# Optimization experiments

Hardware: AMD Instinct MI355X
Metric: run time of the kernel (lower is better)

The kernel has to match this reference:

```python
import jax, jax.numpy as jnp
import numpy as np

# Multi-resolution implicit grid layout (static, mirrors the int32 buffers
# `resolutions` / `offsets` of the torch module).
RESOLUTIONS = (16, 32, 48, 64)
LEVEL_SIZES = tuple(r ** 3 for r in RESOLUTIONS)  # offsets[l+1]-offsets[l]
N_TOTAL = sum(LEVEL_SIZES)  # 409600
B, C_IN, C_OUT, K = 4, 16, 16, 3


def setup_inputs() -> dict:
    key = jax.random.key(0)
    k1, k2, k3 = jax.random.split(key, 3)
    inp = jax.random.normal(k1, (B, N_TOTAL, C_IN), dtype=jnp.float32)
    weight = jax.random.normal(k2, (C_OUT, C_IN, K, K, K), dtype=jnp.float32) * 0.05
    bias = jax.random.normal(k3, (C_OUT,), dtype=jnp.float32) * 0.05
    return {"input": inp, "weight": weight, "bias": bias}


def reference(input, weight, bias):
    """Offset-indexed multi-resolution 3D conv.

    input:  [B, N_total, Cin] flat per-level voxel features,
            level l occupies a contiguous block of resolutions[l]**3 rows
            laid out as a dense R x R x R grid (row-major).
    weight: [Cout, Cin, k, k, k]; bias: [Cout].
    Each level is convolved independently with SAME padding (zero pad at
    level boundaries), then written back to the same flat layout.
    """
    Bv, _, Cin = input.shape
    Cout = weight.shape[0]
    outs = []
    start = 0
    for R in RESOLUTIONS:  # fixed small number of levels
        n = R ** 3
        # [B, n, Cin] -> [B, Cin, R, R, R]
        x = input[:, start:start + n, :].reshape(Bv, R, R, R, Cin)
        x = jnp.transpose(x, (0, 4, 1, 2, 3))
        y = jax.lax.conv_general_dilated(
            x, weight,
            window_strides=(1, 1, 1),
            padding='SAME',
            dimension_numbers=('NCDHW', 'OIDHW', 'NCDHW'),
        )
        y = y + bias[None, :, None, None, None]
        # back to flat layout [B, n, Cout]
        outs.append(jnp.transpose(y, (0, 2, 3, 4, 1)).reshape(Bv, n, Cout))
        start += n
    return jnp.concatenate(outs, axis=1)  # [B, N_total, Cout]
```

## Files before the change

kernel.cpp:

```cpp
#include <hip/hip_runtime.h>

#define N_TOTAL 409600

typedef short short8 __attribute__((ext_vector_type(8)));
typedef float floatx4 __attribute__((ext_vector_type(4)));

__device__ __forceinline__ unsigned short f2bf(float f) {
    unsigned u = __float_as_uint(f);
    u += 0x7fffu + ((u >> 16) & 1u);
    return (unsigned short)(u >> 16);
}

__global__ __launch_bounds__(256) void wt_pack(const float* __restrict__ w,
                                               unsigned short* __restrict__ wtf) {
    int i = blockIdx.x * 256 + threadIdx.x;
    if (i >= 7168) return;
    int j    = i & 7;
    int lane = (i >> 3) & 63;
    int p    = i >> 9;
    int q    = lane >> 4;
    int tap  = 2 * p + (q >> 1);
    int ci   = (q & 1) * 8 + j;
    int co   = lane & 15;
    float v  = (tap < 27) ? w[(co * 16 + ci) * 27 + tap] : 0.0f;
    wtf[(p * 64 + lane) * 8 + j] = f2bf(v);
}

template <int R>
__global__ __launch_bounds__(256) void pad_bf16(const float* __restrict__ in,
                                                unsigned short* __restrict__ dst,
                                                int vbase) {
    constexpr int Rp   = R + 2;
    constexpr int nPad = Rp * Rp * Rp;
    int tid = blockIdx.x * 256 + threadIdx.x;
    if (tid >= nPad * 2) return;
    int half = tid & 1;
    int p    = tid >> 1;
    int b    = blockIdx.y;
    int pw = p % Rp, ph = (p / Rp) % Rp, pd = p / (Rp * Rp);

    short8 o = {0, 0, 0, 0, 0, 0, 0, 0};
    if (pw >= 1 && pw <= R && ph >= 1 && ph <= R && pd >= 1 && pd <= R) {
        int v = (((pd - 1) * R) + (ph - 1)) * R + (pw - 1);
        const float* src = in + ((size_t)(b * N_TOTAL + vbase) + v) * 16 + half * 8;
        float4 a0 = ((const float4*)src)[0];
        float4 a1 = ((const float4*)src)[1];
        o[0] = (short)f2bf(a0.x); o[1] = (short)f2bf(a0.y);
        o[2] = (short)f2bf(a0.z); o[3] = (short)f2bf(a0.w);
        o[4] = (short)f2bf(a1.x); o[5] = (short)f2bf(a1.y);
        o[6] = (short)f2bf(a1.z); o[7] = (short)f2bf(a1.w);
    }
    *(short8*)(dst + ((size_t)b * nPad + p) * 16 + half * 8) = o;
}

template <int R>
__device__ __forceinline__ constexpr int tapOff(int t) {
    constexpr int Rp = R + 2;
    int kd = t / 9, kh = (t / 3) % 3, kw = t % 3;
    return (((kd - 1) * Rp + (kh - 1)) * Rp + (kw - 1)) * 16;
}

template <int R>
__global__ __launch_bounds__(256) void conv_mfma(const unsigned short* __restrict__ grid,
                                                 const unsigned short* __restrict__ wtf,
                                                 const float* __restrict__ bias,
                                                 float* __restrict__ out,
                                                 int vbase) {
    constexpr int Rp   = R + 2;
    constexpr int nPad = Rp * Rp * Rp;
    const int lane = threadIdx.x & 63;
    const int wave = threadIdx.x >> 6;
    const int b    = blockIdx.y;

    const int tile   = blockIdx.x * 4 + wave;
    const int voxel0 = tile * 16;
    const int d  = voxel0 / (R * R);
    const int h  = (voxel0 / R) % R;
    const int w0 = voxel0 % R;

    const int q      = lane >> 4;
    const int r      = lane & 15;
    const int tapSel = q >> 1;
    const int ciHalf = (q & 1) * 8;

    short8 bf[14];
#pragma unroll
    for (int p = 0; p < 14; ++p)
        bf[p] = *(const short8*)(wtf + (p * 64 + lane) * 8);

    const unsigned short* base =
        grid + (size_t)b * nPad * 16 +
        ((((size_t)(d + 1) * Rp + (h + 1)) * Rp + (w0 + 1)) + r) * 16 + ciHalf;

    const float bv = bias[r];
    floatx4 acc = {bv, bv, bv, bv};

#pragma unroll
    for (int p = 0; p < 14; ++p) {
        const int t1  = (2 * p + 1 < 27) ? 2 * p + 1 : 26;
        const int o0  = tapOff<R>(2 * p);
        const int o1  = tapOff<R>(t1);
        const int off = tapSel ? o1 : o0;
        short8 a = *(const short8*)(base + off);
        acc = __builtin_amdgcn_mfma_f32_16x16x32_bf16(a, bf[p], acc, 0, 0, 0);
    }

    const size_t outBase = ((size_t)b * N_TOTAL + vbase + voxel0) * 16;
#pragma unroll
    for (int j = 0; j < 4; ++j) {
        int row = q * 4 + j;
        out[outBase + (size_t)row * 16 + r] = acc[j];
    }
}

__global__ __launch_bounds__(256) void wt_transpose(const float* __restrict__ w,
                                                    float* __restrict__ wt) {
    int i = blockIdx.x * 256 + threadIdx.x;
    if (i < 6912) {
        int co = i / 432;
        int rr = i - co * 432;
        int ci = rr / 27;
        int tap = rr - ci * 27;
        wt[(tap * 16 + ci) * 16 + co] = w[i];
    }
}

template <int R>
__global__ __launch_bounds__(256) void conv_f32(const float* __restrict__ in,
                                                const float* __restrict__ wt,
                                                const float* __restrict__ bias,
                                                float* __restrict__ out, int base) {
    const int v = blockIdx.x * 256 + threadIdx.x;
    const int b = blockIdx.y;
    const int w = v % R, h = (v / R) % R, d = v / (R * R);
    const size_t lvl = ((size_t)b * N_TOTAL + base) * 16;
    const float* inp = in + lvl;
    float acc[16];
#pragma unroll
    for (int co = 0; co < 16; ++co) acc[co] = bias[co];
    for (int kd = 0; kd < 3; ++kd) {
        const int zd = d + kd - 1;
        if ((unsigned)zd >= (unsigned)R) continue;
        for (int kh = 0; kh < 3; ++kh) {
            const int zh = h + kh - 1;
            if ((unsigned)zh >= (unsigned)R) continue;
#pragma unroll
            for (int kw = 0; kw < 3; ++kw) {
                const int zw = w + kw - 1;
                if ((unsigned)zw >= (unsigned)R) continue;
                const float* src = inp + (size_t)(((zd * R + zh) * R) + zw) * 16;
                const float4* p4 = reinterpret_cast<const float4*>(src);
                float4 q0 = p4[0], q1 = p4[1], q2 = p4[2], q3 = p4[3];
                float x[16] = {q0.x, q0.y, q0.z, q0.w, q1.x, q1.y, q1.z, q1.w,
                               q2.x, q2.y, q2.z, q2.w, q3.x, q3.y, q3.z, q3.w};
                const float* wp = wt + ((kd * 3 + kh) * 3 + kw) * 256;
#pragma unroll
                for (int ci = 0; ci < 16; ++ci)
#pragma unroll
                    for (int co = 0; co < 16; ++co)
                        acc[co] = fmaf(x[ci], wp[ci * 16 + co], acc[co]);
            }
        }
    }
    float* dst = out + lvl + (size_t)v * 16;
    float4* d4 = reinterpret_cast<float4*>(dst);
    d4[0] = make_float4(acc[0], acc[1], acc[2], acc[3]);
    d4[1] = make_float4(acc[4], acc[5], acc[6], acc[7]);
    d4[2] = make_float4(acc[8], acc[9], acc[10], acc[11]);
    d4[3] = make_float4(acc[12], acc[13], acc[14], acc[15]);
}

extern "C" void kernel_launch(void* const* d_in, const int* in_sizes, int n_in,
                              void* d_out, int out_size, void* d_ws, size_t ws_size,
                              hipStream_t stream) {
    const float* in   = (const float*)d_in[0];
    const float* wgt  = (const float*)d_in[1];
    const float* bias = (const float*)d_in[2];
    float* out = (float*)d_out;

    const size_t E16 = 8192;
    const size_t E32 = E16 + (size_t)4 * 5832 * 16;
    const size_t E48 = E32 + (size_t)4 * 39304 * 16;
    const size_t E64 = E48 + (size_t)4 * 125000 * 16;
    const size_t END = E64 + (size_t)4 * 287496 * 16;
    const size_t needed = END * sizeof(unsigned short);

    if (ws_size >= needed) {
        unsigned short* ws16 = (unsigned short*)d_ws;
        unsigned short* wtf = ws16;
        unsigned short* g16 = ws16 + E16;
        unsigned short* g32 = ws16 + E32;
        unsigned short* g48 = ws16 + E48;
        unsigned short* g64 = ws16 + E64;

        wt_pack<<<28, 256, 0, stream>>>(wgt, wtf);
        pad_bf16<16><<<dim3(46,   4), 256, 0, stream>>>(in, g16, 0);
        pad_bf16<32><<<dim3(308,  4), 256, 0, stream>>>(in, g32, 4096);
        pad_bf16<48><<<dim3(977,  4), 256, 0, stream>>>(in, g48, 36864);
        pad_bf16<64><<<dim3(2247, 4), 256, 0, stream>>>(in, g64, 147456);

        conv_mfma<16><<<dim3(64,   4), 256, 0, stream>>>(g16, wtf, bias, out, 0);
        conv_mfma<32><<<dim3(512,  4), 256, 0, stream>>>(g32, wtf, bias, out, 4096);
        conv_mfma<48><<<dim3(1728, 4), 256, 0, stream>>>(g48, wtf, bias, out, 36864);
        conv_mfma<64><<<dim3(4096, 4), 256, 0, stream>>>(g64, wtf, bias, out, 147456);
    } else {
        float* wt = (float*)d_ws;
        wt_transpose<<<27, 256, 0, stream>>>(wgt, wt);
        conv_f32<16><<<dim3(16,   4), 256, 0, stream>>>(in, wt, bias, out, 0);
        conv_f32<32><<<dim3(128,  4), 256, 0, stream>>>(in, wt, bias, out, 4096);
        conv_f32<48><<<dim3(432,  4), 256, 0, stream>>>(in, wt, bias, out, 36864);
        conv_f32<64><<<dim3(1024, 4), 256, 0, stream>>>(in, wt, bias, out, 147456);
    }
}
```

Measured before the change: 282.1 us.

## Merge per-level pad and conv launches into two fused kernels, hoist tap loads

Replaces nine launches (weight pack, four pad kernels, four conv kernels) with one pad kernel that also packs weights and one conv kernel. Both dispatch per level by block index. This removes launch gaps and tail underutilisation between the small per-level kernels. The conv body now issues all 14 activation and weight loads up front, behind a sched_barrier, before the MFMA chain, so memory latency overlaps. The cost is higher register pressure, and the weight pack is now done redundantly for each batch index.

```diff
diff --git a/kernel.cpp b/kernel.cpp
--- a/kernel.cpp
+++ b/kernel.cpp
@@ -11,32 +11,21 @@
     return (unsigned short)(u >> 16);
 }
 
-__global__ __launch_bounds__(256) void wt_pack(const float* __restrict__ w,
-                                               unsigned short* __restrict__ wtf) {
-    int i = blockIdx.x * 256 + threadIdx.x;
-    if (i >= 7168) return;
-    int j    = i & 7;
-    int lane = (i >> 3) & 63;
-    int p    = i >> 9;
-    int q    = lane >> 4;
-    int tap  = 2 * p + (q >> 1);
-    int ci   = (q & 1) * 8 + j;
-    int co   = lane & 15;
-    float v  = (tap < 27) ? w[(co * 16 + ci) * 27 + tap] : 0.0f;
-    wtf[(p * 64 + lane) * 8 + j] = f2bf(v);
-}
-
-template <int R>
-__global__ __launch_bounds__(256) void pad_bf16(const float* __restrict__ in,
-                                                unsigned short* __restrict__ dst,
-                                                int vbase) {
-    constexpr int Rp   = R + 2;
+#define E16 8192
+#define E32 (E16 + (size_t)4 * 5832 * 16)
+#define E48 (E32 + (size_t)4 * 39304 * 16)
+#define E64 (E48 + (size_t)4 * 125000 * 16)
+#define EEND (E64 + (size_t)4 * 287496 * 16)
+
+template <int R>
+__device__ __forceinline__ void pad_dev(const float* __restrict__ in,
+                                        unsigned short* __restrict__ dst,
+                                        int vbase, int tid, int b) {
+    constexpr int Rp = R + 2;
     constexpr int nPad = Rp * Rp * Rp;
-    int tid = blockIdx.x * 256 + threadIdx.x;
     if (tid >= nPad * 2) return;
     int half = tid & 1;
-    int p    = tid >> 1;
-    int b    = blockIdx.y;
+    int p = tid >> 1;
     int pw = p % Rp, ph = (p / Rp) % Rp, pd = p / (Rp * Rp);
 
     short8 o = {0, 0, 0, 0, 0, 0, 0, 0};
@@ -53,6 +42,34 @@
     *(short8*)(dst + ((size_t)b * nPad + p) * 16 + half * 8) = o;
 }
 
+__global__ __launch_bounds__(256) void pad_all(const float* __restrict__ in,
+                                               const float* __restrict__ w,
+                                               unsigned short* __restrict__ ws16) {
+    const int bx = blockIdx.x;
+    const int b  = blockIdx.y;
+    if (bx < 46) {
+        pad_dev<16>(in, ws16 + E16, 0, bx * 256 + threadIdx.x, b);
+    } else if (bx < 354) {
+        pad_dev<32>(in, ws16 + E32, 4096, (bx - 46) * 256 + threadIdx.x, b);
+    } else if (bx < 1331) {
+        pad_dev<48>(in, ws16 + E48, 36864, (bx - 354) * 256 + threadIdx.x, b);
+    } else if (bx < 3578) {
+        pad_dev<64>(in, ws16 + E64, 147456, (bx - 1331) * 256 + threadIdx.x, b);
+    } else {
+        int i = (bx - 3578) * 256 + threadIdx.x;
+        if (i >= 7168) return;
+        int j    = i & 7;
+        int lane = (i >> 3) & 63;
+        int p    = i >> 9;
+        int q    = lane >> 4;
+        int tap  = 2 * p + (q >> 1);
+        int ci   = (q & 1) * 8 + j;
+        int co   = lane & 15;
+        float v  = (tap < 27) ? w[(co * 16 + ci) * 27 + tap] : 0.0f;
+        ws16[(p * 64 + lane) * 8 + j] = f2bf(v);
+    }
+}
+
 template <int R>
 __device__ __forceinline__ constexpr int tapOff(int t) {
     constexpr int Rp = R + 2;
@@ -61,18 +78,15 @@
 }
 
 template <int R>
-__global__ __launch_bounds__(256) void conv_mfma(const unsigned short* __restrict__ grid,
-                                                 const unsigned short* __restrict__ wtf,
-                                                 const float* __restrict__ bias,
-                                                 float* __restrict__ out,
-                                                 int vbase) {
-    constexpr int Rp   = R + 2;
+__device__ __forceinline__ void conv_dev(const unsigned short* __restrict__ grid,
+                                         const unsigned short* __restrict__ wtf,
+                                         const float* __restrict__ bias,
+                                         float* __restrict__ out,
+                                         int vbase, int tile, int b) {
+    constexpr int Rp = R + 2;
     constexpr int nPad = Rp * Rp * Rp;
     const int lane = threadIdx.x & 63;
-    const int wave = threadIdx.x >> 6;
-    const int b    = blockIdx.y;
-
-    const int tile   = blockIdx.x * 4 + wave;
+
     const int voxel0 = tile * 16;
     const int d  = voxel0 / (R * R);
     const int h  = (voxel0 / R) % R;
@@ -83,33 +97,53 @@
     const int tapSel = q >> 1;
     const int ciHalf = (q & 1) * 8;
 
-    short8 bf[14];
-#pragma unroll
-    for (int p = 0; p < 14; ++p)
-        bf[p] = *(const short8*)(wtf + (p * 64 + lane) * 8);
-
     const unsigned short* base =
         grid + (size_t)b * nPad * 16 +
         ((((size_t)(d + 1) * Rp + (h + 1)) * Rp + (w0 + 1)) + r) * 16 + ciHalf;
 
+    short8 a[14];
+#pragma unroll
+    for (int p = 0; p < 14; ++p) {
+        const int t1  = (2 * p + 1 < 27) ? 2 * p + 1 : 26;
+        const int off = tapSel ? tapOff<R>(t1) : tapOff<R>(2 * p);
+        a[p] = *(const short8*)(base + off);
+    }
+    short8 bf[14];
+#pragma unroll
+    for (int p = 0; p < 14; ++p)
+        bf[p] = *(const short8*)(wtf + (p * 64 + lane) * 8);
+
+    __builtin_amdgcn_sched_barrier(0);
+
     const float bv = bias[r];
     floatx4 acc = {bv, bv, bv, bv};
-
-#pragma unroll
-    for (int p = 0; p < 14; ++p) {
-        const int t1  = (2 * p + 1 < 27) ? 2 * p + 1 : 26;
-        const int o0  = tapOff<R>(2 * p);
-        const int o1  = tapOff<R>(t1);
-        const int off = tapSel ? o1 : o0;
-        short8 a = *(const short8*)(base + off);
-        acc = __builtin_amdgcn_mfma_f32_16x16x32_bf16(a, bf[p], acc, 0, 0, 0);
-    }
+#pragma unroll
+    for (int p = 0; p < 14; ++p)
+        acc = __builtin_amdgcn_mfma_f32_16x16x32_bf16(a[p], bf[p], acc, 0, 0, 0);
 
     const size_t outBase = ((size_t)b * N_TOTAL + vbase + voxel0) * 16;
 #pragma unroll
     for (int j = 0; j < 4; ++j) {
         int row = q * 4 + j;
         out[outBase + (size_t)row * 16 + r] = acc[j];
+    }
+}
+
+__global__ __launch_bounds__(256, 2) void conv_all(const unsigned short* __restrict__ ws16,
+                                                   const float* __restrict__ bias,
+                                                   float* __restrict__ out) {
+    const int bx   = blockIdx.x;
+    const int b    = blockIdx.y;
+    const int wave = threadIdx.x >> 6;
+    const unsigned short* wtf = ws16;
+    if (bx < 64) {
+        conv_dev<16>(ws16 + E16, wtf, bias, out, 0,      bx * 4 + wave, b);
+    } else if (bx < 576) {
+        conv_dev<32>(ws16 + E32, wtf, bias, out, 4096,   (bx - 64) * 4 + wave, b);
+    } else if (bx < 2304) {
+        conv_dev<48>(ws16 + E48, wtf, bias, out, 36864,  (bx - 576) * 4 + wave, b);
+    } else {
+        conv_dev<64>(ws16 + E64, wtf, bias, out, 147456, (bx - 2304) * 4 + wave, b);
     }
 }
 
@@ -178,31 +212,12 @@
     const float* bias = (const float*)d_in[2];
     float* out = (float*)d_out;
 
-    const size_t E16 = 8192;
-    const size_t E32 = E16 + (size_t)4 * 5832 * 16;
-    const size_t E48 = E32 + (size_t)4 * 39304 * 16;
-    const size_t E64 = E48 + (size_t)4 * 125000 * 16;
-    const size_t END = E64 + (size_t)4 * 287496 * 16;
-    const size_t needed = END * sizeof(unsigned short);
+    const size_t needed = EEND * sizeof(unsigned short);
 
     if (ws_size >= needed) {
         unsigned short* ws16 = (unsigned short*)d_ws;
-        unsigned short* wtf = ws16;
-        unsigned short* g16 = ws16 + E16;
-        unsigned short* g32 = ws16 + E32;
-        unsigned short* g48 = ws16 + E48;
-        unsigned short* g64 = ws16 + E64;
-
-        wt_pack<<<28, 256, 0, stream>>>(wgt, wtf);
-        pad_bf16<16><<<dim3(46,   4), 256, 0, stream>>>(in, g16, 0);
-        pad_bf16<32><<<dim3(308,  4), 256, 0, stream>>>(in, g32, 4096);
-        pad_bf16<48><<<dim3(977,  4), 256, 0, stream>>>(in, g48, 36864);
-        pad_bf16<64><<<dim3(2247, 4), 256, 0, stream>>>(in, g64, 147456);
-
-        conv_mfma<16><<<dim3(64,   4), 256, 0, stream>>>(g16, wtf, bias, out, 0);
-        conv_mfma<32><<<dim3(512,  4), 256, 0, stream>>>(g32, wtf, bias, out, 4096);
-        conv_mfma<48><<<dim3(1728, 4), 256, 0, stream>>>(g48, wtf, bias, out, 36864);
-        conv_mfma<64><<<dim3(4096, 4), 256, 0, stream>>>(g64, wtf, bias, out, 147456);
+        pad_all <<<dim3(3606, 4), 256, 0, stream>>>(in, wgt, ws16);
+        conv_all<<<dim3(6400, 4), 256, 0, stream>>>(ws16, bias, out);
     } else {
         float* wt = (float*)d_ws;
         wt_transpose<<<27, 256, 0, stream>>>(wgt, wt);
```

After: 261.8 us. 7.2% less time.
